# Performance work log

Measured on AMD Instinct MI355X. Metric: run time of the kernel, lower is better.

The kernel has to match this reference:

```python
import jax, jax.numpy as jnp
import numpy as np

N_NODES = 100000
N_EDGES = 1600000
D = 128
NEG_SLOPE = 0.2


def setup_inputs() -> dict:
    key = jax.random.key(0)
    k1, k2, k3, k4, k5, k6 = jax.random.split(key, 6)
    x = jax.random.normal(k1, (N_NODES, D), dtype=jnp.float32)
    src = jax.random.randint(k2, (N_EDGES,), 0, N_NODES)
    dst = jax.random.randint(k3, (N_EDGES,), 0, N_NODES)
    # torch.nn.Linear default init: U(-1/sqrt(fan_in), 1/sqrt(fan_in))
    W = jax.random.uniform(k4, (D, D), dtype=jnp.float32, minval=-1.0, maxval=1.0) / np.sqrt(D)
    a_left = jax.random.uniform(k5, (1, D), dtype=jnp.float32, minval=-1.0, maxval=1.0) / np.sqrt(D)
    a_right = jax.random.uniform(k6, (1, D), dtype=jnp.float32, minval=-1.0, maxval=1.0) / np.sqrt(D)
    return {"x": x, "src": src, "dst": dst, "W": W, "a_left": a_left, "a_right": a_right}


def reference(x, src, dst, W, a_left, a_right):
    n = x.shape[0]
    # node-wise projections
    h = x @ W.T                      # [N, D]
    e_l = h @ a_left.T               # [N, 1]
    e_r = h @ a_right.T              # [N, 1]
    # edge attention logits: u_add_v then leaky_relu
    e = e_l[src] + e_r[dst]          # [E, 1]
    e = jnp.where(e >= 0, e, NEG_SLOPE * e)
    # edge softmax over incoming edges of each destination node
    e = e[:, 0]
    m = jax.ops.segment_max(e, dst, num_segments=n)          # [N]
    m = jnp.where(jnp.isfinite(m), m, 0.0)                   # guard empty segments
    ex = jnp.exp(e - m[dst])                                 # [E]
    denom = jax.ops.segment_sum(ex, dst, num_segments=n)     # [N]
    alpha = ex / jnp.maximum(denom[dst], 1e-38)              # [E]
    # weighted aggregation: sum_e h[src] * alpha -> dst
    msg = h[src] * alpha[:, None]                            # [E, D]
    out = jax.ops.segment_sum(msg, dst, num_segments=n)      # [N, D]
    return out
```

## Files before the change

### kernel.cpp

```cpp
#include <hip/hip_runtime.h>
#include <math.h>

#define N_NODES 100000
#define N_EDGES 1600000
#define D 128
#define NEG_SLOPE_F 0.2f
#define BK 32
#define NB3 3125
#define ECAP 1024
#define BEPB 16384
#define NBINB 98
#define NGEMM 1563
#define DYN_LDS 52224

typedef short short8 __attribute__((ext_vector_type(8)));
typedef float f32x4 __attribute__((ext_vector_type(4)));

__device__ __forceinline__ unsigned short f2bf_rtn(float f) {
    unsigned int u = __float_as_uint(f);
    u += 0x7fffu + ((u >> 16) & 1u);
    return (unsigned short)(u >> 16);
}
__device__ __forceinline__ float bf2f(unsigned short h) {
    return __uint_as_float((unsigned)h << 16);
}

__global__ __launch_bounds__(256) void fused_prep(
        const int* __restrict__ src, const int* __restrict__ dst,
        const float* __restrict__ x, const float* __restrict__ W,
        const float* __restrict__ a_l, const float* __restrict__ a_r,
        unsigned* __restrict__ gcount, unsigned* __restrict__ binned,
        unsigned short* __restrict__ hb, float* __restrict__ e_l,
        float* __restrict__ e_r) {
    extern __shared__ __align__(16) char smem[];
    int tid = threadIdx.x;

    if (blockIdx.x < NBINB) {
        unsigned* hist   = (unsigned*)smem;
        unsigned* startb = hist + NB3;
        unsigned* cnt    = startb + NB3;
        for (int i = tid; i < NB3; i += 256) { hist[i] = 0; cnt[i] = 0; }
        __syncthreads();
        int base = blockIdx.x * BEPB;
        const int4* d4 = (const int4*)dst;
        const int4* s4 = (const int4*)src;
        int i40 = base >> 2;
        for (int it = 0; it < 16; ++it) {
            int i4 = i40 + it * 256 + tid;
            if (i4 * 4 < N_EDGES) {
                int4 v = d4[i4];
                atomicAdd(&hist[v.x >> 5], 1u);
                atomicAdd(&hist[v.y >> 5], 1u);
                atomicAdd(&hist[v.z >> 5], 1u);
                atomicAdd(&hist[v.w >> 5], 1u);
            }
        }
        __syncthreads();
        for (int b = tid; b < NB3; b += 256) {
            unsigned c = hist[b];
            startb[b] = c ? atomicAdd(&gcount[b], c) : 0u;
        }
        __syncthreads();
        for (int it = 0; it < 16; ++it) {
            int i4 = i40 + it * 256 + tid;
            if (i4 * 4 < N_EDGES) {
                int4 dv = d4[i4];
                int4 sv = s4[i4];
#define PUT(dd, ss)                                                          \
                {                                                            \
                    int b = (dd) >> 5;                                       \
                    unsigned r = startb[b] + atomicAdd(&cnt[b], 1u);         \
                    if (r < ECAP)                                            \
                        binned[(size_t)b * ECAP + r] =                       \
                            ((unsigned)((dd) & 31) << 17) | (unsigned)(ss);  \
                }
                PUT(dv.x, sv.x) PUT(dv.y, sv.y) PUT(dv.z, sv.z) PUT(dv.w, sv.w)
#undef PUT
            }
        }
        return;
    }

    unsigned short (*Xh)[136] = (unsigned short(*)[136])smem;
    unsigned short (*Bh)[136] = (unsigned short(*)[136])(smem + 17408);
    unsigned short (*Bl)[136] = (unsigned short(*)[136])(smem + 34816);
    int lane = tid & 63, wid = tid >> 6;
    int p = lane & 15, g = lane >> 4;
    int row0 = (blockIdx.x - NBINB) * 64;
    int n = N_NODES;

    const float4* X4 = (const float4*)x;
    for (int q = 0; q < 8; ++q) {
        int idx = q * 256 + tid;
        int r = idx >> 5, c4 = idx & 31;
        int gr = row0 + r;
        float4 v = (gr < n) ? X4[(size_t)gr * 32 + c4] : make_float4(0.f, 0.f, 0.f, 0.f);
        ushort4 hh;
        hh.x = f2bf_rtn(v.x);
        hh.y = f2bf_rtn(v.y);
        hh.z = f2bf_rtn(v.z);
        hh.w = f2bf_rtn(v.w);
        *(ushort4*)&Xh[r][c4 * 4] = hh;
    }

    f32x4 acc[2][4];
#pragma unroll
    for (int hf = 0; hf < 2; ++hf)
#pragma unroll
        for (int ct = 0; ct < 4; ++ct) acc[hf][ct] = (f32x4)(0.f);

    const float4* W4 = (const float4*)W;
    int arow = wid * 16 + p;

#pragma unroll
    for (int hf = 0; hf < 2; ++hf) {
        __syncthreads();
        for (int q = 0; q < 8; ++q) {
            int idx = q * 256 + tid;
            int r = idx >> 5, c4 = idx & 31;
            float4 v = W4[((size_t)(hf * 64 + r)) * 32 + c4];
            ushort4 hh, ll;
            hh.x = f2bf_rtn(v.x); ll.x = f2bf_rtn(v.x - bf2f(hh.x));
            hh.y = f2bf_rtn(v.y); ll.y = f2bf_rtn(v.y - bf2f(hh.y));
            hh.z = f2bf_rtn(v.z); ll.z = f2bf_rtn(v.z - bf2f(hh.z));
            hh.w = f2bf_rtn(v.w); ll.w = f2bf_rtn(v.w - bf2f(hh.w));
            *(ushort4*)&Bh[r][c4 * 4] = hh;
            *(ushort4*)&Bl[r][c4 * 4] = ll;
        }
        __syncthreads();

#pragma unroll
        for (int kc = 0; kc < 4; ++kc) {
            int cb = kc * 32 + g * 8;
            short8 ah = *(const short8*)&Xh[arow][cb];
#pragma unroll
            for (int ct = 0; ct < 4; ++ct) {
                short8 bh = *(const short8*)&Bh[ct * 16 + p][cb];
                short8 bl = *(const short8*)&Bl[ct * 16 + p][cb];
                acc[hf][ct] = __builtin_amdgcn_mfma_f32_16x16x32_bf16(ah, bh, acc[hf][ct], 0, 0, 0);
                acc[hf][ct] = __builtin_amdgcn_mfma_f32_16x16x32_bf16(ah, bl, acc[hf][ct], 0, 0, 0);
            }
        }
    }

    float al8[2][4], ar8[2][4];
#pragma unroll
    for (int hf = 0; hf < 2; ++hf)
#pragma unroll
        for (int ct = 0; ct < 4; ++ct) {
            al8[hf][ct] = a_l[hf * 64 + ct * 16 + p];
            ar8[hf][ct] = a_r[hf * 64 + ct * 16 + p];
        }
#pragma unroll
    for (int i = 0; i < 4; ++i) {
        int gr = row0 + wid * 16 + g * 4 + i;
        bool ok = gr < n;
        float pl = 0.f, pr = 0.f;
        if (ok) {
#pragma unroll
            for (int hf = 0; hf < 2; ++hf)
#pragma unroll
                for (int ct = 0; ct < 4; ++ct) {
                    float v = acc[hf][ct][i];
                    hb[(size_t)gr * 128 + hf * 64 + ct * 16 + p] = f2bf_rtn(v);
                    pl += v * al8[hf][ct];
                    pr += v * ar8[hf][ct];
                }
        }
#pragma unroll
        for (int o = 8; o; o >>= 1) {
            pl += __shfl_xor(pl, o);
            pr += __shfl_xor(pr, o);
        }
        if (ok && p == 0) { e_l[gr] = pl; e_r[gr] = pr; }
    }
}

__global__ __launch_bounds__(256) void bucket_fused(
        const unsigned short* __restrict__ hb, const float* __restrict__ e_l,
        const float* __restrict__ e_r, const unsigned* __restrict__ gcount,
        const unsigned* __restrict__ binned, float* __restrict__ out) {
    __shared__ unsigned es[ECAP];
    __shared__ float    ee[ECAP];
    __shared__ unsigned short sidx[ECAP];
    __shared__ unsigned cntl[BK];
    __shared__ unsigned startl[BK];
    __shared__ unsigned curl[BK];
    __shared__ float    erl[BK];
    __shared__ int   lds_s[4][64];
    __shared__ float lds_e[4][64];

    int tid = threadIdx.x, lane = tid & 63, w = tid >> 6;
    int g = lane >> 4, p = lane & 15;
    int b = blockIdx.x, d0 = b * BK;
    size_t rs = (size_t)b * ECAP;
    int cnt = min((int)gcount[b], ECAP);

    if (tid < BK) {
        int d = d0 + tid;
        erl[tid] = (d < N_NODES) ? e_r[d] : 0.f;
        cntl[tid] = 0u;
    }
    __syncthreads();

#define ACC8(hv, xe)                                                        \
    acc[0] += xe * __uint_as_float(hv.x << 16);                             \
    acc[1] += xe * __uint_as_float(hv.x & 0xffff0000u);                     \
    acc[2] += xe * __uint_as_float(hv.y << 16);                             \
    acc[3] += xe * __uint_as_float(hv.y & 0xffff0000u);                     \
    acc[4] += xe * __uint_as_float(hv.z << 16);                             \
    acc[5] += xe * __uint_as_float(hv.z & 0xffff0000u);                     \
    acc[6] += xe * __uint_as_float(hv.w << 16);                             \
    acc[7] += xe * __uint_as_float(hv.w & 0xffff0000u);

    for (int i = tid; i < cnt; i += 256) {
        unsigned v = binned[rs + i];
        unsigned ld = v >> 17;
        float e = e_l[v & 0x1ffffu] + erl[ld];
        e = (e >= 0.f) ? e : NEG_SLOPE_F * e;
        es[i] = v;
        ee[i] = __expf(e);
        atomicAdd(&cntl[ld], 1u);
    }
    __syncthreads();
    if (tid < BK) {
        unsigned c = cntl[tid];
        unsigned inc = c;
#pragma unroll
        for (int o = 1; o < BK; o <<= 1) {
            unsigned nv = __shfl_up(inc, o);
            if (lane >= o) inc += nv;
        }
        startl[tid] = inc - c;
        curl[tid] = inc - c;
    }
    __syncthreads();
    for (int i = tid; i < cnt; i += 256) {
        unsigned ld = es[i] >> 17;
        unsigned pos = atomicAdd(&curl[ld], 1u);
        sidx[pos] = (unsigned short)i;
    }
    __syncthreads();
    for (int k = 0; k < BK / 4; ++k) {
        int ld = (k << 2) | w;
        int start = (int)startl[ld];
        int deg = (int)cntl[ld];

        float denom = 0.f;
        float acc[8];
#pragma unroll
        for (int q = 0; q < 8; ++q) acc[q] = 0.f;
        for (int b2 = 0; b2 < deg; b2 += 64) {
            int kk = b2 + lane;
            bool valid = kk < deg;
            int i = valid ? sidx[start + kk] : 0;
            float ex = valid ? ee[i] : 0.f;
            denom += ex;
            lds_s[w][lane] = valid ? (int)(es[i] & 0x1ffffu) : 0;
            lds_e[w][lane] = ex;
            asm volatile("s_waitcnt lgkmcnt(0)" ::: "memory");
            int c2 = min(64, deg - b2);
            int nst = (c2 + 3) >> 2;
            int u = 0;
            for (; u + 4 <= nst; u += 4) {
                int j0 = u * 4 + g;
                int s0 = lds_s[w][j0];       float x0 = lds_e[w][j0];
                int s1 = lds_s[w][j0 + 4];   float x1 = lds_e[w][j0 + 4];
                int s2 = lds_s[w][j0 + 8];   float x2 = lds_e[w][j0 + 8];
                int s3 = lds_s[w][j0 + 12];  float x3 = lds_e[w][j0 + 12];
                uint4 h0 = *(const uint4*)&hb[(size_t)s0 * 128 + p * 8];
                uint4 h1 = *(const uint4*)&hb[(size_t)s1 * 128 + p * 8];
                uint4 h2 = *(const uint4*)&hb[(size_t)s2 * 128 + p * 8];
                uint4 h3 = *(const uint4*)&hb[(size_t)s3 * 128 + p * 8];
                ACC8(h0, x0) ACC8(h1, x1) ACC8(h2, x2) ACC8(h3, x3)
            }
            for (; u < nst; ++u) {
                int j = u * 4 + g;
                int sj = lds_s[w][j];
                float xj = lds_e[w][j];
                uint4 hv = *(const uint4*)&hb[(size_t)sj * 128 + p * 8];
                ACC8(hv, xj)
            }
        }
#pragma unroll
        for (int q = 0; q < 8; ++q) {
            acc[q] += __shfl_xor(acc[q], 16);
            acc[q] += __shfl_xor(acc[q], 32);
        }
#pragma unroll
        for (int o = 32; o; o >>= 1) denom += __shfl_xor(denom, o);
        float inv = 1.f / fmaxf(denom, 1e-38f);
        int d = d0 + ld;
        if (g == 0 && d < N_NODES) {
            f32x4 o0 = {acc[0] * inv, acc[1] * inv, acc[2] * inv, acc[3] * inv};
            f32x4 o1 = {acc[4] * inv, acc[5] * inv, acc[6] * inv, acc[7] * inv};
            __builtin_nontemporal_store(o0, (f32x4*)&out[(size_t)d * 128 + p * 8]);
            __builtin_nontemporal_store(o1, (f32x4*)&out[(size_t)d * 128 + p * 8 + 4]);
        }
    }
#undef ACC8
}

extern "C" void kernel_launch(void* const* d_in, const int* in_sizes, int n_in,
                              void* d_out, int out_size, void* d_ws, size_t ws_size,
                              hipStream_t stream) {
    const float* x   = (const float*)d_in[0];
    const int*   src = (const int*)d_in[1];
    const int*   dst = (const int*)d_in[2];
    const float* W   = (const float*)d_in[3];
    const float* a_l = (const float*)d_in[4];
    const float* a_r = (const float*)d_in[5];
    float* out = (float*)d_out;

    char* ws = (char*)d_ws;
    unsigned short* hb = (unsigned short*)ws; ws += (size_t)N_NODES * D * 2;
    float*    e_l    = (float*)ws;    ws += (size_t)N_NODES * 4;
    float*    e_r    = (float*)ws;    ws += (size_t)N_NODES * 4;
    unsigned* gcount = (unsigned*)ws; ws += (size_t)NB3 * 4;
    unsigned* binned = (unsigned*)ws; ws += (size_t)NB3 * ECAP * 4;

    hipMemsetAsync(gcount, 0, (size_t)NB3 * 4, stream);

    fused_prep<<<NBINB + NGEMM, 256, DYN_LDS, stream>>>(
        src, dst, x, W, a_l, a_r, gcount, binned, hb, e_l, e_r);
    bucket_fused<<<NB3, 256, 0, stream>>>(hb, e_l, e_r, gcount, binned, out);
}
```

Before: 117.2 us.

## Load GEMM A-fragments directly to registers and use direct global atomics for binning

The GEMM blocks now read each wave's x rows straight from global memory into registers as bf16 MFMA A-fragments, dropping the Xh LDS tile and shrinking dynamic LDS from 52 KB to 34 KB, which may allow more resident blocks. The binning blocks drop the LDS histogram pass and per-bin global reservation, and instead take one global atomicAdd per edge on gcount. This removes a pass over dst and several barriers, but adds heavy global atomic contention (1.6M atomics onto 3125 counters). It also changes the order of edges within each bin.

```diff
diff --git a/kernel.cpp b/kernel.cpp
--- a/kernel.cpp
+++ b/kernel.cpp
@@ -11,7 +11,7 @@
 #define BEPB 16384
 #define NBINB 98
 #define NGEMM 1563
-#define DYN_LDS 52224
+#define DYN_LDS 34816
 
 typedef short short8 __attribute__((ext_vector_type(8)));
 typedef float f32x4 __attribute__((ext_vector_type(4)));
@@ -36,31 +36,10 @@
     int tid = threadIdx.x;
 
     if (blockIdx.x < NBINB) {
-        unsigned* hist   = (unsigned*)smem;
-        unsigned* startb = hist + NB3;
-        unsigned* cnt    = startb + NB3;
-        for (int i = tid; i < NB3; i += 256) { hist[i] = 0; cnt[i] = 0; }
-        __syncthreads();
         int base = blockIdx.x * BEPB;
         const int4* d4 = (const int4*)dst;
         const int4* s4 = (const int4*)src;
         int i40 = base >> 2;
-        for (int it = 0; it < 16; ++it) {
-            int i4 = i40 + it * 256 + tid;
-            if (i4 * 4 < N_EDGES) {
-                int4 v = d4[i4];
-                atomicAdd(&hist[v.x >> 5], 1u);
-                atomicAdd(&hist[v.y >> 5], 1u);
-                atomicAdd(&hist[v.z >> 5], 1u);
-                atomicAdd(&hist[v.w >> 5], 1u);
-            }
-        }
-        __syncthreads();
-        for (int b = tid; b < NB3; b += 256) {
-            unsigned c = hist[b];
-            startb[b] = c ? atomicAdd(&gcount[b], c) : 0u;
-        }
-        __syncthreads();
         for (int it = 0; it < 16; ++it) {
             int i4 = i40 + it * 256 + tid;
             if (i4 * 4 < N_EDGES) {
@@ -69,7 +48,7 @@
 #define PUT(dd, ss)                                                          \
                 {                                                            \
                     int b = (dd) >> 5;                                       \
-                    unsigned r = startb[b] + atomicAdd(&cnt[b], 1u);         \
+                    unsigned r = atomicAdd(&gcount[b], 1u);                  \
                     if (r < ECAP)                                            \
                         binned[(size_t)b * ECAP + r] =                       \
                             ((unsigned)((dd) & 31) << 17) | (unsigned)(ss);  \
@@ -81,26 +60,36 @@
         return;
     }
 
-    unsigned short (*Xh)[136] = (unsigned short(*)[136])smem;
-    unsigned short (*Bh)[136] = (unsigned short(*)[136])(smem + 17408);
-    unsigned short (*Bl)[136] = (unsigned short(*)[136])(smem + 34816);
+    unsigned short (*Bh)[136] = (unsigned short(*)[136])smem;
+    unsigned short (*Bl)[136] = (unsigned short(*)[136])(smem + 17408);
     int lane = tid & 63, wid = tid >> 6;
     int p = lane & 15, g = lane >> 4;
     int row0 = (blockIdx.x - NBINB) * 64;
     int n = N_NODES;
 
+    int arow = row0 + wid * 16 + p;
+    int arow_c = min(arow, n - 1);
     const float4* X4 = (const float4*)x;
-    for (int q = 0; q < 8; ++q) {
-        int idx = q * 256 + tid;
-        int r = idx >> 5, c4 = idx & 31;
-        int gr = row0 + r;
-        float4 v = (gr < n) ? X4[(size_t)gr * 32 + c4] : make_float4(0.f, 0.f, 0.f, 0.f);
-        ushort4 hh;
-        hh.x = f2bf_rtn(v.x);
-        hh.y = f2bf_rtn(v.y);
-        hh.z = f2bf_rtn(v.z);
-        hh.w = f2bf_rtn(v.w);
-        *(ushort4*)&Xh[r][c4 * 4] = hh;
+    float4 xa0[4], xa1[4];
+#pragma unroll
+    for (int kc = 0; kc < 4; ++kc) {
+        size_t bi = (size_t)arow_c * 32 + kc * 8 + g * 2;
+        xa0[kc] = X4[bi];
+        xa1[kc] = X4[bi + 1];
+    }
+    short8 ah[4];
+#pragma unroll
+    for (int kc = 0; kc < 4; ++kc) {
+        short8 a;
+        a[0] = (short)f2bf_rtn(xa0[kc].x);
+        a[1] = (short)f2bf_rtn(xa0[kc].y);
+        a[2] = (short)f2bf_rtn(xa0[kc].z);
+        a[3] = (short)f2bf_rtn(xa0[kc].w);
+        a[4] = (short)f2bf_rtn(xa1[kc].x);
+        a[5] = (short)f2bf_rtn(xa1[kc].y);
+        a[6] = (short)f2bf_rtn(xa1[kc].z);
+        a[7] = (short)f2bf_rtn(xa1[kc].w);
+        ah[kc] = a;
     }
 
     f32x4 acc[2][4];
@@ -110,7 +99,6 @@
         for (int ct = 0; ct < 4; ++ct) acc[hf][ct] = (f32x4)(0.f);
 
     const float4* W4 = (const float4*)W;
-    int arow = wid * 16 + p;
 
 #pragma unroll
     for (int hf = 0; hf < 2; ++hf) {
@@ -132,13 +120,12 @@
 #pragma unroll
         for (int kc = 0; kc < 4; ++kc) {
             int cb = kc * 32 + g * 8;
-            short8 ah = *(const short8*)&Xh[arow][cb];
 #pragma unroll
             for (int ct = 0; ct < 4; ++ct) {
                 short8 bh = *(const short8*)&Bh[ct * 16 + p][cb];
                 short8 bl = *(const short8*)&Bl[ct * 16 + p][cb];
-                acc[hf][ct] = __builtin_amdgcn_mfma_f32_16x16x32_bf16(ah, bh, acc[hf][ct], 0, 0, 0);
-                acc[hf][ct] = __builtin_amdgcn_mfma_f32_16x16x32_bf16(ah, bl, acc[hf][ct], 0, 0, 0);
+                acc[hf][ct] = __builtin_amdgcn_mfma_f32_16x16x32_bf16(ah[kc], bh, acc[hf][ct], 0, 0, 0);
+                acc[hf][ct] = __builtin_amdgcn_mfma_f32_16x16x32_bf16(ah[kc], bl, acc[hf][ct], 0, 0, 0);
             }
         }
     }
```

Measured after the change: 220.7 us. +88.2%, slower.
